# Optimization experiments

Hardware: AMD Instinct MI355X
Metric: run time of the kernel (lower is better)

Reference implementation:

```python
import jax, jax.numpy as jnp
from jax import lax
import numpy as np
import math

D = 256  # pyramid feature_size

def _conv(x, w, b, stride, pad):
    y = lax.conv_general_dilated(x, w, (stride, stride), [(pad, pad), (pad, pad)],
                                 dimension_numbers=('NCHW', 'OIHW', 'NCHW'))
    return y + b[None, :, None, None]

def _pe(L, d=D):
    pos = np.arange(L, dtype=np.float32)[:, None]
    div = np.exp(np.arange(0, d, 2, dtype=np.float32) * (-math.log(10000.0) / float(d)))
    pe = np.zeros((L, d), np.float32)
    pe[:, 0::2] = np.sin(pos * div)
    pe[:, 1::2] = np.cos(pos * div)
    return jnp.asarray(pe)

def _up_nearest(x, H, W):
    hi = jnp.arange(H) * x.shape[2] // H
    wi = jnp.arange(W) * x.shape[3] // W
    return x[:, :, hi][:, :, :, wi]

def setup_inputs() -> dict:
    key = jax.random.key(0)
    ks = jax.random.split(key, 24)
    rn = lambda k, s, std=1.0: jax.random.normal(k, s, jnp.float32) * std
    B, S = 8, 5
    z = lambda: jnp.zeros((D,), jnp.float32)
    return {
        'C3': rn(ks[0], (B, 512, 40, 40)),
        'C4': rn(ks[1], (B, 1024, 20, 20)),
        'C5': rn(ks[2], (B, 2048, 10, 10)),
        'S3': rn(ks[3], (B * S, 512, 40, 40)),
        'S4': rn(ks[4], (B * S, 1024, 20, 20)),
        'S5': rn(ks[5], (B * S, 2048, 10, 10)),
        'p3_1_w': rn(ks[6], (D, 512, 1, 1), 0.02), 'p3_1_b': z(),
        'p3_2_w': rn(ks[7], (D, D, 3, 3), 0.02), 'p3_2_b': z(),
        'p4_1_w': rn(ks[8], (D, 1024, 1, 1), 0.02), 'p4_1_b': z(),
        'p4_2_w': rn(ks[9], (D, D, 3, 3), 0.02), 'p4_2_b': z(),
        'p5_1_w': rn(ks[10], (D, 2048, 1, 1), 0.02), 'p5_1_b': z(),
        'p5_2_w': rn(ks[11], (D, D, 3, 3), 0.02), 'p5_2_b': z(),
        'p6_w': rn(ks[12], (D, 2048, 3, 3), 0.02), 'p6_b': z(),
        'p7_w': rn(ks[13], (D, D, 3, 3), 0.02), 'p7_b': z(),
        'q_w': rn(ks[14], (D, D), 0.01), 'q_b': z(),
        'k_w': rn(ks[15], (D, D), 0.01), 'k_b': z(),
    }

def reference(C3, C4, C5, S3, S4, S5,
              p3_1_w, p3_1_b, p3_2_w, p3_2_b,
              p4_1_w, p4_1_b, p4_2_w, p4_2_b,
              p5_1_w, p5_1_b, p5_2_w, p5_2_b,
              p6_w, p6_b, p7_w, p7_b, q_w, q_b, k_w, k_b):
    B = C3.shape[0]
    S = S3.shape[0] // B
    # FPN lateral 1x1 convs (query and support share weights)
    P5x = _conv(C5, p5_1_w, p5_1_b, 1, 0)
    P4x = _conv(C4, p4_1_w, p4_1_b, 1, 0)
    P3x = _conv(C3, p3_1_w, p3_1_b, 1, 0)
    P5s = _conv(S5, p5_1_w, p5_1_b, 1, 0)
    P4s = _conv(S4, p4_1_w, p4_1_b, 1, 0)
    P3s = _conv(S3, p3_1_w, p3_1_b, 1, 0)
    P6x = _conv(C5, p6_w, p6_b, 2, 1)
    P7x = _conv(jax.nn.relu(P6x), p7_w, p7_b, 2, 1)
    P6s = _conv(S5, p6_w, p6_b, 2, 1)
    P7s = _conv(jax.nn.relu(P6s), p7_w, p7_b, 2, 1)
    # top-down pathway (order matches torch source)
    P5u = _up_nearest(P5x, P4x.shape[2], P4x.shape[3])
    P5x = _conv(P5x, p5_2_w, p5_2_b, 1, 1)
    P4x = P5u + P4x
    P4u = _up_nearest(P4x, P3x.shape[2], P3x.shape[3])
    P4x = _conv(P4x, p4_2_w, p4_2_b, 1, 1)
    P3x = _conv(P3x + P4u, p3_2_w, p3_2_b, 1, 1)

    def to_shots(t):  # [B*S,C,H,W] -> [S,B,C,H,W]
        return t.reshape(B, S, t.shape[1], t.shape[2], t.shape[3]).transpose(1, 0, 2, 3, 4)

    qs = [P3x, P4x, P5x, P6x, P7x]
    ss = [to_shots(P3s), to_shots(P4s), to_shots(P5s), to_shots(P6s), to_shots(P7s)]
    outs = []
    scale = math.sqrt(float(D))
    for qx, sx in zip(qs, ss):
        H, W = qx.shape[2], qx.shape[3]
        q = qx.reshape(B, D, H * W).transpose(0, 2, 1)           # [B, HW, D]
        Q = q @ q_w.T + q_b
        L = sx.shape[3] * sx.shape[4]
        s = sx.reshape(S, B, D, L).transpose(0, 1, 3, 2) + _pe(L)  # [S, B, L, D]
        K = s @ k_w.T + k_b
        att = jax.nn.softmax(jnp.einsum('bqd,sbkd->sbqk', Q, K) / scale, axis=-1)
        m = jnp.einsum('sbqk,sbkd->bqd', att, s) / S              # mean over shots fused
        outs.append(jnp.concatenate([qx, m.transpose(0, 2, 1).reshape(B, D, H, W)], axis=1))
    return tuple(outs)
```

## Files before the change

### kernel.cpp

```cpp
#include <hip/hip_runtime.h>
#include <hip/hip_bf16.h>
#include <math.h>

#define LK 72

typedef __hip_bfloat16 bf16;
typedef __bf16 bf16x8 __attribute__((ext_vector_type(8)));
typedef __bf16 bf16x4v __attribute__((ext_vector_type(4)));
typedef float  f32x4  __attribute__((ext_vector_type(4)));

__global__ __launch_bounds__(256)
void pe_init_kernel(float* __restrict__ peT) {
    const int d = blockIdx.x;
    const int j = d >> 1;
    const double dv = exp(-(double)(2 * j) * 9.210340371976184 / 256.0);
    for (int l = threadIdx.x; l < 1600; l += 256) {
        const float arg = (float)l * (float)dv;
        peT[(size_t)d * 1600 + l] = (d & 1) ? cosf(arg) : sinf(arg);
    }
}

__global__ void repack_w(const float* __restrict__ w, __bf16* __restrict__ dst,
                         int Cin, int ksq)
{
    const int total = 256 * Cin * ksq;
    const int idx = blockIdx.x * 256 + threadIdx.x;
    if (idx >= total) return;
    const int o = idx / (Cin * ksq);
    const int r = idx - o * Cin * ksq;
    const int c = r / ksq;
    const int sh = r - c * ksq;
    dst[((size_t)sh * 256 + o) * Cin + c] = (__bf16)w[idx];
}

__global__ void addpe_kernel(const bf16* __restrict__ s, const float* __restrict__ peT,
                             bf16* __restrict__ spe, int L, int total)
{
    const int idx = blockIdx.x * 256 + threadIdx.x;
    if (idx >= total) return;
    const int l = idx % L;
    const int c = (idx / L) & 255;
    spe[idx] = __float2bfloat16(__bfloat162float(s[idx]) + peT[(size_t)c * 1600 + l]);
}

__global__ void bias_init_kernel(float* __restrict__ out, const float* __restrict__ bias,
                                 int N, int total)
{
    const int idx = blockIdx.x * 256 + threadIdx.x;
    if (idx >= total) return;
    out[idx] = bias[(idx / N) & 255];
}

__global__ void cast_f32_bf16(const float* __restrict__ src, bf16* __restrict__ dst,
                              int total)
{
    const int idx = blockIdx.x * 256 + threadIdx.x;
    if (idx < total) dst[idx] = __float2bfloat16(src[idx]);
}

__global__ __launch_bounds__(256)
void gemm1x1_mfma(const void* __restrict__ in, const __bf16* __restrict__ wbf,
                  const float* __restrict__ bias, void* __restrict__ out,
                  int Cin, int N, int in_bf16, int out_mode)
{
    const int b  = blockIdx.z;
    const int o0 = blockIdx.y * 64;
    const int n0 = blockIdx.x * 64;
    const int t  = threadIdx.x;
    const int wv  = t >> 6;
    const int ln  = t & 63;
    const int lm  = ln & 15;
    const int kq8 = (ln >> 4) * 8;

    __shared__ __bf16 Bs[64][LK];

    f32x4 acc[4];
    #pragma unroll
    for (int ct = 0; ct < 4; ++ct) acc[ct] = (f32x4){0.f, 0.f, 0.f, 0.f};

    const int cg = t >> 4;
    const int ng = t & 15;
    const int nb = n0 + ng * 4;
    const bool vec_ok = ((N & 3) == 0) && (nb + 3 < N);

    const float*  inf = (const float*)in;
    const __bf16* inh = (const __bf16*)in;
    const size_t inb0 = (size_t)b * Cin * N;

    const __bf16* arow = wbf + (size_t)(o0 + wv * 16 + lm) * Cin;

    for (int c0 = 0; c0 < Cin; c0 += 64) {
        __syncthreads();
        float rv[4][4];
        #pragma unroll
        for (int i = 0; i < 4; ++i) {
            const int c = c0 + cg * 4 + i;
            const size_t base = inb0 + (size_t)c * N + nb;
            if (vec_ok) {
                if (in_bf16) {
                    const bf16x4v v = *(const bf16x4v*)&inh[base];
                    rv[i][0] = (float)v[0]; rv[i][1] = (float)v[1];
                    rv[i][2] = (float)v[2]; rv[i][3] = (float)v[3];
                } else {
                    const float4 v = *(const float4*)&inf[base];
                    rv[i][0] = v.x; rv[i][1] = v.y; rv[i][2] = v.z; rv[i][3] = v.w;
                }
            } else {
                #pragma unroll
                for (int jj = 0; jj < 4; ++jj) {
                    const int n = nb + jj;
                    rv[i][jj] = (n < N) ? (in_bf16 ? (float)inh[inb0 + (size_t)c * N + n]
                                                   : inf[inb0 + (size_t)c * N + n])
                                        : 0.f;
                }
            }
        }
        #pragma unroll
        for (int jj = 0; jj < 4; ++jj) {
            bf16x4v pk;
            pk[0] = (__bf16)rv[0][jj]; pk[1] = (__bf16)rv[1][jj];
            pk[2] = (__bf16)rv[2][jj]; pk[3] = (__bf16)rv[3][jj];
            *(bf16x4v*)&Bs[ng * 4 + jj][cg * 4] = pk;
        }
        __syncthreads();

        #pragma unroll
        for (int k0 = 0; k0 < 64; k0 += 32) {
            const bf16x8 a = *(const bf16x8*)&arow[c0 + k0 + kq8];
            #pragma unroll
            for (int ct = 0; ct < 4; ++ct) {
                const bf16x8 bb = *(const bf16x8*)&Bs[ct * 16 + lm][k0 + kq8];
                acc[ct] = __builtin_amdgcn_mfma_f32_16x16x32_bf16(a, bb, acc[ct], 0, 0, 0);
            }
        }
    }

    const int rbase = o0 + wv * 16 + (ln >> 4) * 4;
    #pragma unroll
    for (int ct = 0; ct < 4; ++ct) {
        const int col = n0 + ct * 16 + lm;
        if (col < N) {
            if (out_mode == 2) {
                bf16x4v pk;
                #pragma unroll
                for (int r = 0; r < 4; ++r)
                    pk[r] = (__bf16)(acc[ct][r] + bias[rbase + r]);
                *(bf16x4v*)&((__bf16*)out)[((size_t)b * N + col) * 256 + rbase] = pk;
            } else {
                const size_t outb = (size_t)b * 256 * N;
                #pragma unroll
                for (int r = 0; r < 4; ++r) {
                    const int o = rbase + r;
                    const float val = acc[ct][r] + bias[o];
                    if (out_mode == 1) ((__bf16*)out)[outb + (size_t)o * N + col] = (__bf16)val;
                    else               ((float*)out)[outb + (size_t)o * N + col] = val;
                }
            }
        }
    }
}

__global__ __launch_bounds__(256)
void conv3x3h_mfma(const void* __restrict__ in, const __bf16* __restrict__ wbf,
                   const float* __restrict__ bias, void* __restrict__ out,
                   const float* __restrict__ addup,
                   int Cin, int H, int W, int in_bf16, int out_bf16)
{
    const int b  = blockIdx.z;
    const int o0 = blockIdx.y * 64;
    const int n0 = blockIdx.x * 64;
    const int N  = H * W;
    const int EXT = 64 + 2 * W + 2;
    const int t  = threadIdx.x;
    const int wv = t >> 6;
    const int ln = t & 63;
    const int lm = ln & 15;
    const int kq8 = (ln >> 4) * 8;

    __shared__ __bf16 Bs[146][LK];

    f32x4 acc[4];
    #pragma unroll
    for (int ct = 0; ct < 4; ++ct) acc[ct] = (f32x4){0.f, 0.f, 0.f, 0.f};

    const size_t inb0 = (size_t)b * Cin * N;
    const int upH = H >> 1, upW = W >> 1;
    const float* addb = addup ? addup + (size_t)b * Cin * upH * upW : nullptr;
    const float*  inf = (const float*)in;
    const __bf16* inh = (const __bf16*)in;

    int yct[4], xct[4];
    bool nok[4];
    #pragma unroll
    for (int ct = 0; ct < 4; ++ct) {
        const int n = n0 + ct * 16 + lm;
        nok[ct] = n < N;
        yct[ct] = nok[ct] ? n / W : 0;
        xct[ct] = nok[ct] ? n - yct[ct] * W : 0;
    }

    bf16x8 zro;
    #pragma unroll
    for (int j = 0; j < 8; ++j) zro[j] = (__bf16)0.f;

    const int srow = t & 63;
    const int kb16 = (t >> 6) * 16;
    const int basep = n0 - W - 1;

    for (int c0 = 0; c0 < Cin; c0 += 64) {
        __syncthreads();
        for (int rb = 0; rb < EXT; rb += 64) {
            const int row = rb + srow;
            if (row < EXT) {
                const int p = basep + row;
                const bool ok = (p >= 0) && (p < N);
                const int py = ok ? p / W : 0;
                const int px = ok ? p - py * W : 0;
                #pragma unroll
                for (int j = 0; j < 16; ++j) {
                    const int kk = kb16 + j;
                    const int c  = c0 + kk;
                    float v = 0.f;
                    if (ok) {
                        v = in_bf16 ? (float)inh[inb0 + (size_t)c * N + p]
                                    : inf[inb0 + (size_t)c * N + p];
                        if (addb) v += addb[((size_t)c * upH + (py >> 1)) * upW + (px >> 1)];
                    }
                    Bs[row][kk] = (__bf16)v;
                }
            }
        }
        __syncthreads();

        #pragma unroll
        for (int sh = 0; sh < 9; ++sh) {
            const int ky = sh / 3, kx = sh - ky * 3;
            const int off = (ky - 1) * W + (kx - 1) + W + 1;
            bool vm[4];
            #pragma unroll
            for (int ct = 0; ct < 4; ++ct)
                vm[ct] = nok[ct] && (unsigned)(yct[ct] + ky - 1) < (unsigned)H
                                 && (unsigned)(xct[ct] + kx - 1) < (unsigned)W;
            const __bf16* ash = wbf + ((size_t)sh * 256 + o0 + wv * 16 + lm) * Cin + c0;
            #pragma unroll
            for (int k0 = 0; k0 < 64; k0 += 32) {
                const bf16x8 a = *(const bf16x8*)&ash[k0 + kq8];
                #pragma unroll
                for (int ct = 0; ct < 4; ++ct) {
                    bf16x8 bb = *(const bf16x8*)&Bs[ct * 16 + lm + off][k0 + kq8];
                    bb = vm[ct] ? bb : zro;
                    acc[ct] = __builtin_amdgcn_mfma_f32_16x16x32_bf16(a, bb, acc[ct], 0, 0, 0);
                }
            }
        }
    }

    const size_t outb = (size_t)b * 256 * N;
    const int rbase = o0 + wv * 16 + (ln >> 4) * 4;
    #pragma unroll
    for (int ct = 0; ct < 4; ++ct) {
        const int col = n0 + ct * 16 + lm;
        if (col < N) {
            #pragma unroll
            for (int r = 0; r < 4; ++r) {
                const int o = rbase + r;
                const float val = acc[ct][r] + bias[o];
                if (out_bf16) ((__bf16*)out)[outb + (size_t)o * N + col] = (__bf16)val;
                else          ((float*)out)[outb + (size_t)o * N + col] = val;
            }
        }
    }
}

__global__ __launch_bounds__(256)
void convsk_mfma(const void* __restrict__ in, const __bf16* __restrict__ wbf,
                 float* __restrict__ out,
                 int B, int Cin, int Hin, int Win, int Ho, int Wo,
                 int ks, int stride, int pad, int relu_in, int in_bf16,
                 int kchunk)
{
    const int N  = Ho * Wo;
    const int NT = B * N;
    const int col0 = blockIdx.x * 64;
    const int t  = threadIdx.x;
    const int wv = t >> 6;
    const int ln = t & 63;
    const int lm = ln & 15;
    const int kq8 = (ln >> 4) * 8;

    __shared__ __bf16 Bs[64][LK];

    f32x4 acc[4][4];
    #pragma unroll
    for (int rt = 0; rt < 4; ++rt)
        #pragma unroll
        for (int ct = 0; ct < 4; ++ct) acc[rt][ct] = (f32x4){0.f, 0.f, 0.f, 0.f};

    const size_t inHW = (size_t)Hin * Win;
    const int ksq = ks * ks;
    const float*  inf = (const float*)in;
    const __bf16* inh = (const __bf16*)in;

    const int srow = t & 63;
    const int kb16 = (t >> 6) * 16;
    const int scol = col0 + srow;
    const bool cvalid = scol < NT;
    int sb = 0, yo = 0, xo = 0;
    if (cvalid) {
        sb = scol / N;
        const int sn = scol - sb * N;
        yo = sn / Wo; xo = sn - yo * Wo;
    }

    const int Ktot = Cin * ksq;
    const int kbeg = blockIdx.y * kchunk;
    const int kend = min(kbeg + kchunk, Ktot);

    for (int k0 = kbeg; k0 < kend; k0 += 64) {
        const int sh = k0 / Cin;
        const int c0 = k0 - sh * Cin;
        const int ky = sh / ks, kx = sh - ky * ks;
        const int iy = yo * stride + ky - pad;
        const int ix = xo * stride + kx - pad;
        const bool ld_ok = cvalid && iy >= 0 && iy < Hin && ix >= 0 && ix < Win;
        const size_t sidx = (size_t)sb * Cin * inHW + (size_t)iy * Win + ix;

        __syncthreads();
        #pragma unroll
        for (int j = 0; j < 16; ++j) {
            const int kk = kb16 + j;
            const int c  = c0 + kk;
            float v = 0.f;
            if (ld_ok) {
                v = in_bf16 ? (float)inh[sidx + (size_t)c * inHW]
                            : inf[sidx + (size_t)c * inHW];
                if (relu_in) v = fmaxf(v, 0.f);
            }
            Bs[srow][kk] = (__bf16)v;
        }
        __syncthreads();

        #pragma unroll
        for (int k32 = 0; k32 < 64; k32 += 32) {
            bf16x8 bfr[4];
            #pragma unroll
            for (int ct = 0; ct < 4; ++ct)
                bfr[ct] = *(const bf16x8*)&Bs[ct * 16 + lm][k32 + kq8];
            #pragma unroll
            for (int rt = 0; rt < 4; ++rt) {
                const __bf16* ap = wbf + ((size_t)sh * 256 + wv * 64 + rt * 16 + lm) * Cin
                                       + c0 + k32 + kq8;
                const bf16x8 a = *(const bf16x8*)ap;
                #pragma unroll
                for (int ct = 0; ct < 4; ++ct)
                    acc[rt][ct] = __builtin_amdgcn_mfma_f32_16x16x32_bf16(a, bfr[ct],
                                                                          acc[rt][ct], 0, 0, 0);
            }
        }
    }

    const int rb0 = wv * 64 + (ln >> 4) * 4;
    #pragma unroll
    for (int ct = 0; ct < 4; ++ct) {
        const int col = col0 + ct * 16 + lm;
        if (col < NT) {
            const int be = col / N;
            const int ne = col - be * N;
            float* ob = out + (size_t)be * 256 * N + ne;
            #pragma unroll
            for (int rt = 0; rt < 4; ++rt)
                #pragma unroll
                for (int r = 0; r < 4; ++r)
                    atomicAdd(&ob[(size_t)(rb0 + rt * 16 + r) * N], acc[rt][ct][r]);
        }
    }
}

__global__ void add_up_kernel(const float* __restrict__ a, const float* __restrict__ up,
                              float* __restrict__ o, int H, int W, int total)
{
    const int idx = blockIdx.x * 256 + threadIdx.x;
    if (idx >= total) return;
    const int x = idx % W;
    const int tmp = idx / W;
    const int y = tmp % H;
    const int bc = tmp / H;
    o[idx] = a[idx] + up[((size_t)bc * (H >> 1) + (y >> 1)) * (W >> 1) + (x >> 1)];
}

__global__ __launch_bounds__(256)
void attn_mfma(const __bf16* __restrict__ Qrow, const __bf16* __restrict__ Krow,
               const bf16* __restrict__ Sv, float* __restrict__ outp, int L, int S)
{
    const int bs = blockIdx.x;
    const int b  = bs / 5;
    const int s  = bs - b * 5;
    const int q0 = blockIdx.y * 64;
    const int t  = threadIdx.x;
    const int wv = t >> 6;
    const int ln = t & 63;
    const int lm = ln & 15;
    const int lg = ln >> 4;

    __shared__ __bf16 Ks[32][264];
    __shared__ __bf16 Vt[256][40];
    __shared__ __bf16 Pl[4][16][40];

    bf16x8 qf[8];
    {
        const int q = q0 + wv * 16 + lm;
        if (q < L) {
            const __bf16* qp = Qrow + ((size_t)b * L + q) * 256 + lg * 8;
            #pragma unroll
            for (int sl = 0; sl < 8; ++sl) qf[sl] = *(const bf16x8*)&qp[sl * 32];
        } else {
            #pragma unroll
            for (int sl = 0; sl < 8; ++sl)
                #pragma unroll
                for (int j = 0; j < 8; ++j) qf[sl][j] = (__bf16)0.f;
        }
    }

    f32x4 acc[16];
    #pragma unroll
    for (int ds = 0; ds < 16; ++ds) acc[ds] = (f32x4){0.f, 0.f, 0.f, 0.f};
    float m_run[4] = {-INFINITY, -INFINITY, -INFINITY, -INFINITY};
    float l_run[4] = {0.f, 0.f, 0.f, 0.f};

    const size_t kbase = (size_t)(b * S + s) * L * 256;
    const __bf16* vb0  = (const __bf16*)Sv + (size_t)(b * S + s) * 256 * L;

    const int krow_ = t >> 3;
    const int kcb   = (t & 7) * 32;
    const __bf16* vsrc0 = vb0 + (size_t)t * L;

    bf16x8 kr[4], vr[4];
    bf16x8 zro;
    #pragma unroll
    for (int j = 0; j < 8; ++j) zro[j] = (__bf16)0.f;

    auto load_tile = [&](int l0) {
        const int l = l0 + krow_;
        if (l < L) {
            const __bf16* src = Krow + kbase + (size_t)l * 256 + kcb;
            #pragma unroll
            for (int j = 0; j < 4; ++j) kr[j] = *(const bf16x8*)&src[j * 8];
        } else {
            #pragma unroll
            for (int j = 0; j < 4; ++j) kr[j] = zro;
        }
        const __bf16* src = vsrc0 + l0;
        if (l0 + 32 <= L && ((((size_t)src) & 15) == 0)) {
            #pragma unroll
            for (int j = 0; j < 4; ++j) vr[j] = *(const bf16x8*)&src[j * 8];
        } else {
            #pragma unroll
            for (int j = 0; j < 4; ++j) {
                #pragma unroll
                for (int e = 0; e < 8; ++e) {
                    const int l = l0 + j * 8 + e;
                    vr[j][e] = (l < L) ? src[j * 8 + e] : (__bf16)0.f;
                }
            }
        }
    };

    const int nt = (L + 31) >> 5;
    load_tile(0);

    for (int lt = 0; lt < nt; ++lt) {
        __syncthreads();
        #pragma unroll
        for (int j = 0; j < 4; ++j) *(bf16x8*)&Ks[krow_][kcb + j * 8] = kr[j];
        #pragma unroll
        for (int j = 0; j < 4; ++j) *(bf16x8*)&Vt[t][j * 8] = vr[j];
        if (lt + 1 < nt) load_tile((lt + 1) << 5);
        __syncthreads();

        const int l0 = lt << 5;

        f32x4 sc0 = (f32x4){0.f, 0.f, 0.f, 0.f};
        f32x4 sc1 = (f32x4){0.f, 0.f, 0.f, 0.f};
        #pragma unroll
        for (int sl = 0; sl < 8; ++sl) {
            const bf16x8 k0 = *(const bf16x8*)&Ks[lm][sl * 32 + lg * 8];
            const bf16x8 k1 = *(const bf16x8*)&Ks[16 + lm][sl * 32 + lg * 8];
            sc0 = __builtin_amdgcn_mfma_f32_16x16x32_bf16(qf[sl], k0, sc0, 0, 0, 0);
            sc1 = __builtin_amdgcn_mfma_f32_16x16x32_bf16(qf[sl], k1, sc1, 0, 0, 0);
        }

        const bool v0 = (l0 + lm) < L;
        const bool v1 = (l0 + 16 + lm) < L;
        float p0[4], p1[4], mt[4];
        #pragma unroll
        for (int r = 0; r < 4; ++r) {
            const float a = v0 ? sc0[r] * 0.0625f : -INFINITY;
            const float c = v1 ? sc1[r] * 0.0625f : -INFINITY;
            p0[r] = a; p1[r] = c; mt[r] = fmaxf(a, c);
        }
        #pragma unroll
        for (int w = 1; w < 16; w <<= 1)
            #pragma unroll
            for (int r = 0; r < 4; ++r) mt[r] = fmaxf(mt[r], __shfl_xor(mt[r], w, 16));

        bool nochange = true;
        #pragma unroll
        for (int r = 0; r < 4; ++r) nochange = nochange && (mt[r] <= m_run[r]);
        const bool skip = __all(nochange);

        float mn[4], rs[4];
        #pragma unroll
        for (int r = 0; r < 4; ++r) {
            mn[r] = skip ? m_run[r] : fmaxf(m_run[r], mt[r]);
            p0[r] = v0 ? __expf(p0[r] - mn[r]) : 0.f;
            p1[r] = v1 ? __expf(p1[r] - mn[r]) : 0.f;
            rs[r] = p0[r] + p1[r];
        }
        #pragma unroll
        for (int w = 1; w < 16; w <<= 1)
            #pragma unroll
            for (int r = 0; r < 4; ++r) rs[r] += __shfl_xor(rs[r], w, 16);

        if (skip) {
            #pragma unroll
            for (int r = 0; r < 4; ++r) l_run[r] += rs[r];
        } else {
            float alpha[4];
            #pragma unroll
            for (int r = 0; r < 4; ++r) {
                alpha[r] = __expf(m_run[r] - mn[r]);
                l_run[r] = l_run[r] * alpha[r] + rs[r];
                m_run[r] = mn[r];
            }
            #pragma unroll
            for (int ds = 0; ds < 16; ++ds)
                #pragma unroll
                for (int r = 0; r < 4; ++r) acc[ds][r] *= alpha[r];
        }

        #pragma unroll
        for (int r = 0; r < 4; ++r) {
            Pl[wv][lg * 4 + r][lm]      = (__bf16)p0[r];
            Pl[wv][lg * 4 + r][16 + lm] = (__bf16)p1[r];
        }
        const bf16x8 pa = *(const bf16x8*)&Pl[wv][lm][lg * 8];

        #pragma unroll
        for (int ds = 0; ds < 16; ++ds) {
            const bf16x8 vv = *(const bf16x8*)&Vt[ds * 16 + lm][lg * 8];
            acc[ds] = __builtin_amdgcn_mfma_f32_16x16x32_bf16(pa, vv, acc[ds], 0, 0, 0);
        }
    }

    const int qrow = q0 + wv * 16 + lg * 4;
    float inv[4];
    #pragma unroll
    for (int r = 0; r < 4; ++r) inv[r] = 1.f / (l_run[r] * (float)S);
    #pragma unroll
    for (int ds = 0; ds < 16; ++ds) {
        const int d = ds * 16 + lm;
        float* ob = outp + ((size_t)b * 512 + 256 + d) * L;
        #pragma unroll
        for (int r = 0; r < 4; ++r) {
            const int q = qrow + r;
            if (q < L) atomicAdd(&ob[q], acc[ds][r] * inv[r]);
        }
    }
}

__global__ void zero_attn_half(float* __restrict__ outp, int L, int total)
{
    const int idx = blockIdx.x * 256 + threadIdx.x;
    if (idx >= total) return;
    const int b = idx / (256 * L);
    const int r = idx - b * 256 * L;
    outp[((size_t)b * 512 + 256) * L + r] = 0.f;
}

__global__ void copy_cast_kernel(const void* __restrict__ src, float* __restrict__ dst,
                                 int HW, int total, int in_bf16)
{
    const int idx = blockIdx.x * 256 + threadIdx.x;
    if (idx >= total) return;
    const int b = idx / (256 * HW);
    const int r = idx - b * 256 * HW;
    const float v = in_bf16 ? __bfloat162float(((const bf16*)src)[idx])
                            : ((const float*)src)[idx];
    dst[(size_t)b * 512 * HW + r] = v;
}

extern "C" void kernel_launch(void* const* d_in, const int* in_sizes, int n_in,
                              void* d_out, int out_size, void* d_ws, size_t ws_size,
                              hipStream_t stream)
{
    (void)in_sizes; (void)n_in; (void)out_size; (void)ws_size;
    const float* C3 = (const float*)d_in[0];
    const float* C4 = (const float*)d_in[1];
    const float* C5 = (const float*)d_in[2];
    const float* S3 = (const float*)d_in[3];
    const float* S4 = (const float*)d_in[4];
    const float* S5 = (const float*)d_in[5];
    const float* p31w = (const float*)d_in[6];  const float* p31b = (const float*)d_in[7];
    const float* p32w = (const float*)d_in[8];  const float* p32b = (const float*)d_in[9];
    const float* p41w = (const float*)d_in[10]; const float* p41b = (const float*)d_in[11];
    const float* p42w = (const float*)d_in[12]; const float* p42b = (const float*)d_in[13];
    const float* p51w = (const float*)d_in[14]; const float* p51b = (const float*)d_in[15];
    const float* p52w = (const float*)d_in[16]; const float* p52b = (const float*)d_in[17];
    const float* p6w  = (const float*)d_in[18]; const float* p6b  = (const float*)d_in[19];
    const float* p7w  = (const float*)d_in[20]; const float* p7b  = (const float*)d_in[21];
    const float* qw   = (const float*)d_in[22]; const float* qb   = (const float*)d_in[23];
    const float* kw   = (const float*)d_in[24]; const float* kb   = (const float*)d_in[25];
    float* out = (float*)d_out;

    uint8_t* base = (uint8_t*)d_ws;
    size_t off = 0;
    auto A = [&](size_t bytes) { size_t r = off; off += (bytes + 255) & ~(size_t)255; return r; };
    float* pPE  = (float*)(base + A((size_t)256 * 1600 * 4));
    bf16*  pP3q = (bf16*) (base + A((size_t)8  * 256 * 1600 * 2));
    float* pP4q = (float*)(base + A((size_t)8  * 256 * 400  * 4));
    float* pP5q = (float*)(base + A((size_t)8  * 256 * 100  * 4));
    bf16*  pP3s = (bf16*) (base + A((size_t)40 * 256 * 1600 * 2));
    bf16*  pP4s = (bf16*) (base + A((size_t)40 * 256 * 400  * 2));
    bf16*  pP5s = (bf16*) (base + A((size_t)40 * 256 * 100  * 2));
    float* pP6q = (float*)(base + A((size_t)8  * 256 * 25   * 4));
    float* pP7q = (float*)(base + A((size_t)8  * 256 * 9    * 4));
    float* pP6sF= (float*)(base + A((size_t)40 * 256 * 25   * 4));
    float* pP7sF= (float*)(base + A((size_t)40 * 256 * 9    * 4));
    bf16*  pP6s = (bf16*) (base + A((size_t)40 * 256 * 25   * 2));
    bf16*  pP7s = (bf16*) (base + A((size_t)40 * 256 * 9    * 2));
    float* pP4m = (float*)(base + A((size_t)8  * 256 * 400  * 4));
    float* pP5f = (float*)(base + A((size_t)8  * 256 * 100  * 4));
    float* pP4f = (float*)(base + A((size_t)8  * 256 * 400  * 4));
    bf16*  pP3f = (bf16*) (base + A((size_t)8  * 256 * 1600 * 2));
    __bf16* pQ  = (__bf16*)(base + A((size_t)8  * 1600 * 256 * 2));
    __bf16* pK  = (__bf16*)(base + A((size_t)40 * 1600 * 256 * 2));
    bf16*  pSPE = (bf16*) (base + A((size_t)40 * 256 * 1600 * 2));
    __bf16* r31 = (__bf16*)(base + A((size_t)256 * 512 * 2));
    __bf16* r32 = (__bf16*)(base + A((size_t)256 * 256 * 9 * 2));
    __bf16* r41 = (__bf16*)(base + A((size_t)256 * 1024 * 2));
    __bf16* r42 = (__bf16*)(base + A((size_t)256 * 256 * 9 * 2));
    __bf16* r51 = (__bf16*)(base + A((size_t)256 * 2048 * 2));
    __bf16* r52 = (__bf16*)(base + A((size_t)256 * 256 * 9 * 2));
    __bf16* r6  = (__bf16*)(base + A((size_t)256 * 2048 * 9 * 2));
    __bf16* r7  = (__bf16*)(base + A((size_t)256 * 256 * 9 * 2));
    __bf16* rq  = (__bf16*)(base + A((size_t)256 * 256 * 2));
    __bf16* rk  = (__bf16*)(base + A((size_t)256 * 256 * 2));

    pe_init_kernel<<<dim3(256), dim3(256), 0, stream>>>(pPE);

    auto rep = [&](const float* w, __bf16* dst, int Cin, int ksq) {
        const int total = 256 * Cin * ksq;
        repack_w<<<dim3((total + 255) / 256), dim3(256), 0, stream>>>(w, dst, Cin, ksq);
    };
    rep(p31w, r31, 512, 1);  rep(p32w, r32, 256, 9);
    rep(p41w, r41, 1024, 1); rep(p42w, r42, 256, 9);
    rep(p51w, r51, 2048, 1); rep(p52w, r52, 256, 9);
    rep(p6w,  r6,  2048, 9); rep(p7w,  r7,  256, 9);
    rep(qw,   rq,  256, 1);  rep(kw,   rk,  256, 1);

    auto g1 = [&](const void* in, const __bf16* wbf, const float* bias, void* o,
                  int B, int Cin, int N, int in_bf16, int out_mode) {
        dim3 g((N + 63) / 64, 4, B);
        gemm1x1_mfma<<<g, dim3(256), 0, stream>>>(in, wbf, bias, o, Cin, N,
                                                  in_bf16, out_mode);
    };
    auto ch3 = [&](const void* in, const __bf16* wbf, const float* bias, void* o,
                   int B, int Cin, int H, int W, const float* addup,
                   int in_bf16, int out_bf16) {
        const int N = H * W;
        dim3 g((N + 63) / 64, 4, B);
        conv3x3h_mfma<<<g, dim3(256), 0, stream>>>(in, wbf, bias, o, addup,
                                                   Cin, H, W, in_bf16, out_bf16);
    };
    auto csk = [&](const void* in, const __bf16* wbf, const float* bias, float* o,
                   int B, int Cin, int Hin, int Win, int Ho, int Wo,
                   int stride, int pad, int relu_in, int in_bf16, int kchunk) {
        const int N = Ho * Wo;
        const int NT = B * N;
        const int Ktot = Cin * 9;
        const int total = B * 256 * N;
        bias_init_kernel<<<dim3((total + 255) / 256), dim3(256), 0, stream>>>(
            o, bias, N, total);
        dim3 g((NT + 63) / 64, (Ktot + kchunk - 1) / kchunk, 1);
        convsk_mfma<<<g, dim3(256), 0, stream>>>(in, wbf, o, B, Cin, Hin, Win, Ho, Wo,
                                                 3, stride, pad, relu_in, in_bf16, kchunk);
    };

    g1(C3, r31, p31b, pP3q, 8,  512,  1600, 0, 1);
    g1(C4, r41, p41b, pP4q, 8,  1024, 400,  0, 0);
    g1(C5, r51, p51b, pP5q, 8,  2048, 100,  0, 0);
    g1(S3, r31, p31b, pP3s, 40, 512,  1600, 0, 1);
    g1(S4, r41, p41b, pP4s, 40, 1024, 400,  0, 1);
    g1(S5, r51, p51b, pP5s, 40, 2048, 100,  0, 1);
    csk(C5,    r6, p6b, pP6q,  8,  2048, 10, 10, 5, 5, 2, 1, 0, 0, 576);
    csk(S5,    r6, p6b, pP6sF, 40, 2048, 10, 10, 5, 5, 2, 1, 0, 0, 1152);
    {
        const int t6 = 40 * 256 * 25;
        cast_f32_bf16<<<dim3((t6 + 255) / 256), dim3(256), 0, stream>>>(pP6sF, pP6s, t6);
    }
    csk(pP6q,  r7, p7b, pP7q,  8,  256, 5, 5, 3, 3, 2, 1, 1, 0, 576);
    csk(pP6sF, r7, p7b, pP7sF, 40, 256, 5, 5, 3, 3, 2, 1, 1, 0, 576);
    {
        const int t7 = 40 * 256 * 9;
        cast_f32_bf16<<<dim3((t7 + 255) / 256), dim3(256), 0, stream>>>(pP7sF, pP7s, t7);
    }
    {
        const int total = 8 * 256 * 400;
        add_up_kernel<<<dim3((total + 255) / 256), dim3(256), 0, stream>>>(
            pP4q, pP5q, pP4m, 20, 20, total);
    }
    ch3(pP5q, r52, p52b, pP5f, 8, 256, 10, 10, nullptr, 0, 0);
    ch3(pP4m, r42, p42b, pP4f, 8, 256, 20, 20, nullptr, 0, 0);
    ch3(pP3q, r32, p32b, pP3f, 8, 256, 40, 40, pP4m, 1, 1);

    const int Ls[5] = {1600, 400, 100, 25, 9};
    const void* qsrc[5] = {pP3f, pP4f, pP5f, pP6q, pP7q};
    const int   qbf [5] = {1, 0, 0, 0, 0};
    const bf16* ssrc[5] = {pP3s, pP4s, pP5s, pP6s, pP7s};
    size_t ooff[5];
    {
        size_t ao = 0;
        for (int i = 0; i < 5; ++i) { ooff[i] = ao; ao += (size_t)8 * 512 * Ls[i]; }
    }
    for (int i = 0; i < 5; ++i) {
        const int L = Ls[i];
        const int stotal = 40 * 256 * L;
        addpe_kernel<<<dim3((stotal + 255) / 256), dim3(256), 0, stream>>>(
            ssrc[i], pPE, pSPE, L, stotal);
        g1(qsrc[i], rq, qb, pQ, 8, 256, L, qbf[i], 2);
        g1(pSPE, rk, kb, pK, 40, 256, L, 1, 2);
        const int total = 8 * 256 * L;
        zero_attn_half<<<dim3((total + 255) / 256), dim3(256), 0, stream>>>(
            out + ooff[i], L, total);
        attn_mfma<<<dim3(40, (L + 63) / 64), dim3(256), 0, stream>>>(
            pQ, pK, pSPE, out + ooff[i], L, 5);
        copy_cast_kernel<<<dim3((total + 255) / 256), dim3(256), 0, stream>>>(
            qsrc[i], out + ooff[i], L, total, qbf[i]);
    }
}
```

Baseline: 2.182 ms.

## Swizzle V tile in LDS and drop register prefetch of K/V tiles

Applies an XOR swizzle to the column blocks of the transposed V tile in shared memory so the 16-row MFMA operand reads hit different banks. It also removes the register double-buffer prefetch, so each K/V tile is now loaded from global and stored to LDS inside the loop. This cuts register pressure, which may help occupancy, but global load latency is no longer overlapped with the previous tile's compute.

```diff
diff --git a/kernel.cpp b/kernel.cpp
--- a/kernel.cpp
+++ b/kernel.cpp
@@ -429,55 +429,45 @@
 
     const size_t kbase = (size_t)(b * S + s) * L * 256;
     const __bf16* vb0  = (const __bf16*)Sv + (size_t)(b * S + s) * 256 * L;
-
-    const int krow_ = t >> 3;
-    const int kcb   = (t & 7) * 32;
-    const __bf16* vsrc0 = vb0 + (size_t)t * L;
-
-    bf16x8 kr[4], vr[4];
-    bf16x8 zro;
-    #pragma unroll
-    for (int j = 0; j < 8; ++j) zro[j] = (__bf16)0.f;
-
-    auto load_tile = [&](int l0) {
-        const int l = l0 + krow_;
-        if (l < L) {
-            const __bf16* src = Krow + kbase + (size_t)l * 256 + kcb;
-            #pragma unroll
-            for (int j = 0; j < 4; ++j) kr[j] = *(const bf16x8*)&src[j * 8];
-        } else {
-            #pragma unroll
-            for (int j = 0; j < 4; ++j) kr[j] = zro;
-        }
-        const __bf16* src = vsrc0 + l0;
-        if (l0 + 32 <= L && ((((size_t)src) & 15) == 0)) {
-            #pragma unroll
-            for (int j = 0; j < 4; ++j) vr[j] = *(const bf16x8*)&src[j * 8];
-        } else {
-            #pragma unroll
-            for (int j = 0; j < 4; ++j) {
-                #pragma unroll
-                for (int e = 0; e < 8; ++e) {
-                    const int l = l0 + j * 8 + e;
-                    vr[j][e] = (l < L) ? src[j * 8 + e] : (__bf16)0.f;
+    const int vswz = (t >> 3) & 3;
+
+    const int nt = (L + 31) >> 5;
+    for (int lt = 0; lt < nt; ++lt) {
+        const int l0 = lt << 5;
+        __syncthreads();
+        {
+            const int row = t >> 3, cb = (t & 7) * 32;
+            const int l = l0 + row;
+            if (l < L) {
+                const __bf16* src = Krow + kbase + (size_t)l * 256 + cb;
+                #pragma unroll
+                for (int j = 0; j < 4; ++j)
+                    *(bf16x8*)&Ks[row][cb + j * 8] = *(const bf16x8*)&src[j * 8];
+            } else {
+                #pragma unroll
+                for (int j = 0; j < 32; ++j) Ks[row][cb + j] = (__bf16)0.f;
+            }
+        }
+        {
+            const __bf16* src = vb0 + (size_t)t * L + l0;
+            if (l0 + 32 <= L && ((((size_t)src) & 15) == 0)) {
+                #pragma unroll
+                for (int j = 0; j < 4; ++j)
+                    *(bf16x8*)&Vt[t][(j ^ vswz) * 8] = *(const bf16x8*)&src[j * 8];
+            } else {
+                #pragma unroll
+                for (int j = 0; j < 4; ++j) {
+                    bf16x8 v;
+                    #pragma unroll
+                    for (int e = 0; e < 8; ++e) {
+                        const int l = l0 + j * 8 + e;
+                        v[e] = (l < L) ? src[j * 8 + e] : (__bf16)0.f;
+                    }
+                    *(bf16x8*)&Vt[t][(j ^ vswz) * 8] = v;
                 }
             }
         }
-    };
-
-    const int nt = (L + 31) >> 5;
-    load_tile(0);
-
-    for (int lt = 0; lt < nt; ++lt) {
         __syncthreads();
-        #pragma unroll
-        for (int j = 0; j < 4; ++j) *(bf16x8*)&Ks[krow_][kcb + j * 8] = kr[j];
-        #pragma unroll
-        for (int j = 0; j < 4; ++j) *(bf16x8*)&Vt[t][j * 8] = vr[j];
-        if (lt + 1 < nt) load_tile((lt + 1) << 5);
-        __syncthreads();
-
-        const int l0 = lt << 5;
 
         f32x4 sc0 = (f32x4){0.f, 0.f, 0.f, 0.f};
         f32x4 sc1 = (f32x4){0.f, 0.f, 0.f, 0.f};
@@ -547,7 +537,8 @@
 
         #pragma unroll
         for (int ds = 0; ds < 16; ++ds) {
-            const bf16x8 vv = *(const bf16x8*)&Vt[ds * 16 + lm][lg * 8];
+            const int row = ds * 16 + lm;
+            const bf16x8 vv = *(const bf16x8*)&Vt[row][(lg ^ ((row >> 3) & 3)) * 8];
             acc[ds] = __builtin_amdgcn_mfma_f32_16x16x32_bf16(pa, vv, acc[ds], 0, 0, 0);
         }
     }
```

Result: slower. 2.270 ms (+4.0%).
